# Optimization experiments

Hardware: AMD Instinct MI355X
Metric: run time of the kernel (lower is better)

Reference implementation:

```python
import jax, jax.numpy as jnp
import numpy as np

B, L, K = 4096, 4096, 10


def _sparsemax(z):
    # z: [..., n]; Martins & Astudillo sparsemax along last dim
    n = z.shape[-1]
    zs = -jnp.sort(-z, axis=-1)                      # descending
    cum = jnp.cumsum(zs, axis=-1)
    r = jnp.arange(1, n + 1, dtype=z.dtype)
    support = (1.0 + r * zs) > cum                   # [..., n]
    ksel = jnp.sum(support, axis=-1, keepdims=True)  # support size
    tau = (jnp.take_along_axis(cum, ksel - 1, axis=-1) - 1.0) / ksel.astype(z.dtype)
    return jnp.maximum(z - tau, 0.0)


def _topk_bitvectors(logits, k):
    # k highest-scoring binary vectors z in {0,1}^L under <z, logits>
    # (faithful to the CPU batched_topk: detached logits)
    lg = jax.lax.stop_gradient(logits)
    b, latent = lg.shape
    base = (lg > 0).astype(lg.dtype)                 # argmax config [B, L]
    costs = jnp.abs(lg)                              # flip costs
    neg_small, pos = jax.lax.top_k(-costs, k)        # k smallest costs + positions
    c_small = -neg_small                             # [B, k]
    m = 1 << k                                       # 2^k candidate flip subsets
    bits = ((jnp.arange(m)[:, None] >> jnp.arange(k)[None, :]) & 1).astype(lg.dtype)  # [2^k, k]
    sums = jnp.einsum('mk,bk->bm', bits, c_small)    # total flip cost per subset
    _, best = jax.lax.top_k(-sums, k)                # k cheapest subsets [B, k]
    flips = bits[best]                               # [B, k, k] which small-cost bits to flip
    base_at = jnp.take_along_axis(base, pos, axis=1) # base bit value at flip positions [B, k]
    delta = flips * (1.0 - 2.0 * base_at[:, None, :])  # +1 or -1 where flipped
    bv = jnp.broadcast_to(base[:, None, :], (b, k, latent))
    bidx = jnp.arange(b)[:, None, None]
    cidx = jnp.arange(k)[None, :, None]
    jpos = pos[:, None, :]                           # [B, 1, k]
    bv = bv.at[bidx, cidx, jpos].add(delta)          # scatter flips -> [B, k, L]
    return bv


def reference(logits, k):
    bv = _topk_bitvectors(logits, k)                         # [B, k, L]
    scores = jnp.einsum('bkj,bj->bk', bv, logits)            # [B, k]
    distr = _sparsemax(scores)                               # [B, k]
    p = distr.reshape(-1)
    safe_p = jnp.where(p > 0, p, 1.0)
    entropy = -jnp.sum(jnp.where(p > 0, p * jnp.log(safe_p), 0.0))
    batch_size = logits.shape[0]
    return bv, distr, entropy / batch_size


def setup_inputs() -> dict:
    key = jax.random.key(0)
    logits = jax.random.normal(key, (B, L), dtype=jnp.float32)
    return {"logits": logits, "k": K}
```

## Files before the change

kernel.cpp:

```cpp
#include <hip/hip_runtime.h>
#include <stdint.h>

#define NB   4096
#define LDIM 4096
#define KK   10
#define TPB  256

__global__ __launch_bounds__(TPB) void topk_sparsemax(
    const float* __restrict__ logits,
    float* __restrict__ bv,
    float* __restrict__ distr,
    float* __restrict__ ent)
{
    __shared__ unsigned long long s_red[4];
    __shared__ float s_wsum[4];
    __shared__ float s_csmall[KK];
    __shared__ int   s_pos[KK];
    __shared__ int   s_sign[KK];
    __shared__ int   s_bestm[KK];
    __shared__ float s_cost[KK];

    const int b    = blockIdx.x;
    const int t    = threadIdx.x;
    const int lane = t & 63;
    const int wv   = t >> 6;
    const float* __restrict__ row = logits + (size_t)b * LDIM;

    float vals[16];
#pragma unroll
    for (int q = 0; q < 4; q++) {
        const float4 f = *(const float4*)(row + (q << 10) + (t << 2));
        vals[q*4+0] = f.x; vals[q*4+1] = f.y; vals[q*4+2] = f.z; vals[q*4+3] = f.w;
    }

    float s0 = 0.f;
#pragma unroll
    for (int i = 0; i < 16; i++) s0 += vals[i] > 0.f ? vals[i] : 0.f;
#pragma unroll
    for (int off = 1; off < 64; off <<= 1) s0 += __shfl_xor(s0, off, 64);
    if (lane == 0) s_wsum[wv] = s0;
    __syncthreads();
    const float S0 = (s_wsum[0] + s_wsum[1]) + (s_wsum[2] + s_wsum[3]);

    unsigned int taken = 0u;
    for (int c = 0; c < KK; c++) {
        unsigned long long best = ~0ull;
#pragma unroll
        for (int i = 0; i < 16; i++) {
            if (!(taken & (1u << i))) {
                const float val  = vals[i];
                const float cost = fabsf(val);
                const int   idx  = ((i >> 2) << 10) + (t << 2) + (i & 3);
                const unsigned long long pk =
                    ((unsigned long long)__float_as_uint(cost) << 32)
                    | (unsigned)((idx << 1) | (val > 0.f ? 1 : 0));
                if (pk < best) best = pk;
            }
        }
#pragma unroll
        for (int off = 1; off < 64; off <<= 1) {
            const unsigned long long o = __shfl_xor(best, off, 64);
            if (o < best) best = o;
        }
        if (lane == 0) s_red[wv] = best;
        __syncthreads();
        unsigned long long w = s_red[0];
        if (s_red[1] < w) w = s_red[1];
        if (s_red[2] < w) w = s_red[2];
        if (s_red[3] < w) w = s_red[3];
        const unsigned lo = (unsigned)w;
        const int widx = (int)(lo >> 1);
        if (t == 0) {
            s_pos[c]    = widx;
            s_sign[c]   = (int)(lo & 1u);
            s_csmall[c] = __uint_as_float((unsigned)(w >> 32));
        }
        const int rem = widx & 1023;
        if ((rem >> 2) == t) taken |= 1u << (((widx >> 10) << 2) | (rem & 3));
        __syncthreads();
    }

    float csm[KK];
#pragma unroll
    for (int j = 0; j < KK; j++) csm[j] = s_csmall[j];
    float sums[4];
#pragma unroll
    for (int i = 0; i < 4; i++) {
        const int m = (t << 2) | i;
        float acc = 0.f;
#pragma unroll
        for (int j = 0; j < KK; j++) acc += (m & (1 << j)) ? csm[j] : 0.f;
        sums[i] = acc;
    }
    unsigned int taken2 = 0u;
    for (int c = 0; c < KK; c++) {
        unsigned long long best = ~0ull;
#pragma unroll
        for (int i = 0; i < 4; i++) {
            if (!(taken2 & (1u << i))) {
                const unsigned long long pk =
                    ((unsigned long long)__float_as_uint(sums[i]) << 32)
                    | (unsigned)((t << 2) | i);
                if (pk < best) best = pk;
            }
        }
#pragma unroll
        for (int off = 1; off < 64; off <<= 1) {
            const unsigned long long o = __shfl_xor(best, off, 64);
            if (o < best) best = o;
        }
        if (lane == 0) s_red[wv] = best;
        __syncthreads();
        unsigned long long w = s_red[0];
        if (s_red[1] < w) w = s_red[1];
        if (s_red[2] < w) w = s_red[2];
        if (s_red[3] < w) w = s_red[3];
        const int wm = (int)(unsigned)w;
        if (t == 0) {
            s_bestm[c] = wm;
            s_cost[c]  = __uint_as_float((unsigned)(w >> 32));
        }
        if ((wm >> 2) == t) taken2 |= 1u << (wm & 3);
        __syncthreads();
    }

    if (t == 0) {
        float z[KK];
#pragma unroll
        for (int c = 0; c < KK; c++) z[c] = S0 - s_cost[c];
        float acc = 0.f; int ks = 0;
#pragma unroll
        for (int r = 1; r <= KK; r++) {
            acc += z[r-1];
            if (1.f + (float)r * z[r-1] > acc) ks++;
        }
        float acc2 = 0.f;
#pragma unroll
        for (int r = 0; r < KK; r++) if (r < ks) acc2 += z[r];
        const float tau = (acc2 - 1.f) / (float)ks;
        float entl = 0.f;
        float* drow = distr + b * KK;
#pragma unroll
        for (int c = 0; c < KK; c++) {
            float p = z[c] - tau;
            p = p > 0.f ? p : 0.f;
            drow[c] = p;
            if (p > 0.f) entl -= p * logf(p);
        }
        atomicAdd(ent, entl * (1.0f / (float)NB));
    }

    float4 base4[4];
#pragma unroll
    for (int q = 0; q < 4; q++) {
        base4[q].x = vals[q*4+0] > 0.f ? 1.f : 0.f;
        base4[q].y = vals[q*4+1] > 0.f ? 1.f : 0.f;
        base4[q].z = vals[q*4+2] > 0.f ? 1.f : 0.f;
        base4[q].w = vals[q*4+3] > 0.f ? 1.f : 0.f;
    }
    float* out0 = bv + (size_t)b * (KK * LDIM);
#pragma unroll
    for (int c = 0; c < KK; c++) {
        float* orow = out0 + c * LDIM + (t << 2);
#pragma unroll
        for (int q = 0; q < 4; q++)
            *(float4*)(orow + (q << 10)) = base4[q];
    }

    __syncthreads();
    if (t < KK * KK) {
        const int c = t / KK, j = t % KK;
        if ((s_bestm[c] >> j) & 1)
            out0[c * LDIM + s_pos[j]] = s_sign[j] ? 0.f : 1.f;
    }
}

extern "C" void kernel_launch(void* const* d_in, const int* in_sizes, int n_in,
                              void* d_out, int out_size, void* d_ws, size_t ws_size,
                              hipStream_t stream)
{
    const float* logits = (const float*)d_in[0];
    float* out   = (float*)d_out;
    float* bv    = out;
    float* distr = out + (size_t)NB * KK * LDIM;
    float* ent   = distr + (size_t)NB * KK;
    hipMemsetAsync(ent, 0, sizeof(float), stream);
    topk_sparsemax<<<dim3(NB), dim3(TPB), 0, stream>>>(logits, bv, distr, ent);
}
```

Baseline: 721.0 us.

## Replace iterative block top-k with threshold candidate filtering and single-wave selection

Replaces the 10 block-wide argmin passes (each with two barriers) with one pass that gathers candidates whose cost falls under an adaptive threshold into shared memory, followed by a single wavefront that picks the 10 smallest from that list. The subset-cost top-k also moves into one wave, with 16 sums per lane and no block barriers, and it now runs after the base bitvector stores are issued so it can overlap them. The goal is to remove the many __syncthreads-heavy reduction rounds. In exchange it adds shared atomics and a retry loop over thresholds, with a fallback that rescans the row from global memory.

```diff
diff --git a/kernel.cpp b/kernel.cpp
--- a/kernel.cpp
+++ b/kernel.cpp
@@ -5,6 +5,16 @@
 #define LDIM 4096
 #define KK   10
 #define TPB  256
+#define CAP  1024
+
+__device__ __forceinline__ unsigned long long wave_min_u64(unsigned long long v) {
+#pragma unroll
+    for (int off = 1; off < 64; off <<= 1) {
+        const unsigned long long o = __shfl_xor(v, off, 64);
+        if (o < v) v = o;
+    }
+    return v;
+}
 
 __global__ __launch_bounds__(TPB) void topk_sparsemax(
     const float* __restrict__ logits,
@@ -12,13 +22,12 @@
     float* __restrict__ distr,
     float* __restrict__ ent)
 {
-    __shared__ unsigned long long s_red[4];
     __shared__ float s_wsum[4];
-    __shared__ float s_csmall[KK];
     __shared__ int   s_pos[KK];
     __shared__ int   s_sign[KK];
     __shared__ int   s_bestm[KK];
-    __shared__ float s_cost[KK];
+    __shared__ int   s_cnt;
+    __shared__ unsigned long long s_cand[CAP];
 
     const int b    = blockIdx.x;
     const int t    = threadIdx.x;
@@ -39,115 +48,30 @@
 #pragma unroll
     for (int off = 1; off < 64; off <<= 1) s0 += __shfl_xor(s0, off, 64);
     if (lane == 0) s_wsum[wv] = s0;
-    __syncthreads();
-    const float S0 = (s_wsum[0] + s_wsum[1]) + (s_wsum[2] + s_wsum[3]);
-
-    unsigned int taken = 0u;
-    for (int c = 0; c < KK; c++) {
-        unsigned long long best = ~0ull;
+
+    float T = 0.02f;
+    int cnt = 0;
+    for (int attempt = 0; attempt < 15; attempt++) {
+        if (t == 0) s_cnt = 0;
+        __syncthreads();
 #pragma unroll
         for (int i = 0; i < 16; i++) {
-            if (!(taken & (1u << i))) {
-                const float val  = vals[i];
-                const float cost = fabsf(val);
-                const int   idx  = ((i >> 2) << 10) + (t << 2) + (i & 3);
+            const float v    = vals[i];
+            const float cost = fabsf(v);
+            if (cost < T) {
+                const int idx = ((i >> 2) << 10) + (t << 2) + (i & 3);
                 const unsigned long long pk =
                     ((unsigned long long)__float_as_uint(cost) << 32)
-                    | (unsigned)((idx << 1) | (val > 0.f ? 1 : 0));
-                if (pk < best) best = pk;
-            }
-        }
-#pragma unroll
-        for (int off = 1; off < 64; off <<= 1) {
-            const unsigned long long o = __shfl_xor(best, off, 64);
-            if (o < best) best = o;
-        }
-        if (lane == 0) s_red[wv] = best;
+                    | (unsigned)((idx << 1) | (v > 0.f ? 1 : 0));
+                const int p = atomicAdd(&s_cnt, 1);
+                if (p < CAP) s_cand[p] = pk;
+            }
+        }
         __syncthreads();
-        unsigned long long w = s_red[0];
-        if (s_red[1] < w) w = s_red[1];
-        if (s_red[2] < w) w = s_red[2];
-        if (s_red[3] < w) w = s_red[3];
-        const unsigned lo = (unsigned)w;
-        const int widx = (int)(lo >> 1);
-        if (t == 0) {
-            s_pos[c]    = widx;
-            s_sign[c]   = (int)(lo & 1u);
-            s_csmall[c] = __uint_as_float((unsigned)(w >> 32));
-        }
-        const int rem = widx & 1023;
-        if ((rem >> 2) == t) taken |= 1u << (((widx >> 10) << 2) | (rem & 3));
+        cnt = s_cnt;
+        if (cnt >= KK && cnt <= CAP) break;
+        T = (cnt < KK) ? T * 4.0f : T * 0.25f;
         __syncthreads();
-    }
-
-    float csm[KK];
-#pragma unroll
-    for (int j = 0; j < KK; j++) csm[j] = s_csmall[j];
-    float sums[4];
-#pragma unroll
-    for (int i = 0; i < 4; i++) {
-        const int m = (t << 2) | i;
-        float acc = 0.f;
-#pragma unroll
-        for (int j = 0; j < KK; j++) acc += (m & (1 << j)) ? csm[j] : 0.f;
-        sums[i] = acc;
-    }
-    unsigned int taken2 = 0u;
-    for (int c = 0; c < KK; c++) {
-        unsigned long long best = ~0ull;
-#pragma unroll
-        for (int i = 0; i < 4; i++) {
-            if (!(taken2 & (1u << i))) {
-                const unsigned long long pk =
-                    ((unsigned long long)__float_as_uint(sums[i]) << 32)
-                    | (unsigned)((t << 2) | i);
-                if (pk < best) best = pk;
-            }
-        }
-#pragma unroll
-        for (int off = 1; off < 64; off <<= 1) {
-            const unsigned long long o = __shfl_xor(best, off, 64);
-            if (o < best) best = o;
-        }
-        if (lane == 0) s_red[wv] = best;
-        __syncthreads();
-        unsigned long long w = s_red[0];
-        if (s_red[1] < w) w = s_red[1];
-        if (s_red[2] < w) w = s_red[2];
-        if (s_red[3] < w) w = s_red[3];
-        const int wm = (int)(unsigned)w;
-        if (t == 0) {
-            s_bestm[c] = wm;
-            s_cost[c]  = __uint_as_float((unsigned)(w >> 32));
-        }
-        if ((wm >> 2) == t) taken2 |= 1u << (wm & 3);
-        __syncthreads();
-    }
-
-    if (t == 0) {
-        float z[KK];
-#pragma unroll
-        for (int c = 0; c < KK; c++) z[c] = S0 - s_cost[c];
-        float acc = 0.f; int ks = 0;
-#pragma unroll
-        for (int r = 1; r <= KK; r++) {
-            acc += z[r-1];
-            if (1.f + (float)r * z[r-1] > acc) ks++;
-        }
-        float acc2 = 0.f;
-#pragma unroll
-        for (int r = 0; r < KK; r++) if (r < ks) acc2 += z[r];
-        const float tau = (acc2 - 1.f) / (float)ks;
-        float entl = 0.f;
-        float* drow = distr + b * KK;
-#pragma unroll
-        for (int c = 0; c < KK; c++) {
-            float p = z[c] - tau;
-            p = p > 0.f ? p : 0.f;
-            drow[c] = p;
-            if (p > 0.f) entl -= p * logf(p);
-        }
-        atomicAdd(ent, entl * (1.0f / (float)NB));
     }
 
     float4 base4[4];
@@ -165,6 +89,104 @@
 #pragma unroll
         for (int q = 0; q < 4; q++)
             *(float4*)(orow + (q << 10)) = base4[q];
+    }
+
+    if (wv == 0) {
+        const float S0 = (s_wsum[0] + s_wsum[1]) + (s_wsum[2] + s_wsum[3]);
+        float csm[KK];
+        unsigned long long prev = 0ull;
+
+        if (cnt >= KK && cnt <= CAP) {
+            const int nc = cnt;
+#pragma unroll
+            for (int c = 0; c < KK; c++) {
+                unsigned long long best = ~0ull;
+                for (int p = lane; p < nc; p += 64) {
+                    const unsigned long long pk = s_cand[p];
+                    if ((c == 0 || pk > prev) && pk < best) best = pk;
+                }
+                best = wave_min_u64(best);
+                prev = best;
+                csm[c] = __uint_as_float((unsigned)(best >> 32));
+                if (lane == 0) {
+                    const unsigned lo = (unsigned)best;
+                    s_pos[c]  = (int)(lo >> 1);
+                    s_sign[c] = (int)(lo & 1u);
+                }
+            }
+        } else {
+#pragma unroll
+            for (int c = 0; c < KK; c++) {
+                unsigned long long best = ~0ull;
+                for (int p = lane; p < LDIM; p += 64) {
+                    const float v    = row[p];
+                    const float cost = fabsf(v);
+                    const unsigned long long pk =
+                        ((unsigned long long)__float_as_uint(cost) << 32)
+                        | (unsigned)((p << 1) | (v > 0.f ? 1 : 0));
+                    if ((c == 0 || pk > prev) && pk < best) best = pk;
+                }
+                best = wave_min_u64(best);
+                prev = best;
+                csm[c] = __uint_as_float((unsigned)(best >> 32));
+                if (lane == 0) {
+                    const unsigned lo = (unsigned)best;
+                    s_pos[c]  = (int)(lo >> 1);
+                    s_sign[c] = (int)(lo & 1u);
+                }
+            }
+        }
+
+        float sums[16];
+#pragma unroll
+        for (int i = 0; i < 16; i++) {
+            const int m = (lane << 4) | i;
+            float acc = 0.f;
+#pragma unroll
+            for (int j = 0; j < KK; j++) acc += (m & (1 << j)) ? csm[j] : 0.f;
+            sums[i] = acc;
+        }
+
+        float zc[KK];
+        unsigned long long prev2 = 0ull;
+#pragma unroll
+        for (int c = 0; c < KK; c++) {
+            unsigned long long best = ~0ull;
+#pragma unroll
+            for (int i = 0; i < 16; i++) {
+                const unsigned long long pk =
+                    ((unsigned long long)__float_as_uint(sums[i]) << 32)
+                    | (unsigned)((lane << 4) | i);
+                if ((c == 0 || pk > prev2) && pk < best) best = pk;
+            }
+            best = wave_min_u64(best);
+            prev2 = best;
+            zc[c] = S0 - __uint_as_float((unsigned)(best >> 32));
+            if (lane == 0) s_bestm[c] = (int)((unsigned)best & 1023u);
+        }
+
+        if (lane == 0) {
+            float acc = 0.f; int ks = 0;
+#pragma unroll
+            for (int r = 1; r <= KK; r++) {
+                acc += zc[r-1];
+                if (1.f + (float)r * zc[r-1] > acc) ks++;
+            }
+            float acc2 = 0.f;
+#pragma unroll
+            for (int r = 0; r < KK; r++) if (r < ks) acc2 += zc[r];
+            const float tau = (acc2 - 1.f) / (float)ks;
+            float entl = 0.f;
+            float* drow = distr + b * KK;
+#pragma unroll
+            for (int c = 0; c < KK; c++) {
+                float p = zc[c] - tau;
+                p = p > 0.f ? p : 0.f;
+                drow[c] = p;
+                if (p > 0.f) entl -= p * logf(p);
+            }
+            atomicAdd(ent, entl * (1.0f / (float)NB));
+        }
     }
 
     __syncthreads();
```

After: 718.0 us. Within noise of the previous version (-0.4%).
